# Performance work log

Hardware: AMD Instinct MI355X
Metric: run time of the kernel (lower is better)

Reference implementation:

```python
import jax, jax.numpy as jnp
import numpy as np


def setup_inputs() -> dict:
    key = jax.random.key(0)
    x = jax.random.normal(key, (4096, 512), dtype=jnp.float32)
    return {"x": x}


def reference(x):
    # Pairwise Euclidean distances for all (i, j) with i > j, flattened in the
    # same order as the original nested loop: (1,0),(2,0),(2,1),(3,0),...
    n = x.shape[0]
    sq = jnp.sum(x * x, axis=1)                      # [N]
    gram = x @ x.T                                   # [N, N]
    d2 = sq[:, None] + sq[None, :] - 2.0 * gram      # [N, N] squared dists
    ii, jj = jnp.tril_indices(n, k=-1)               # row-major lower triangle
    return jnp.sqrt(jnp.maximum(d2[ii, jj], 0.0))    # [N*(N-1)/2]
```

## Files before the change

kernel.cpp:

```cpp
#include <hip/hip_runtime.h>
#include <hip/hip_bf16.h>
#include <stdint.h>

#define N 4096
#define D 512
#define TILE 128
#define BK 128
#define KITERS (D / BK)
#define NB (N / TILE)

typedef float f32x4 __attribute__((ext_vector_type(4)));
typedef int   i32x8 __attribute__((ext_vector_type(8)));
typedef int   i32x4 __attribute__((ext_vector_type(4)));

__global__ __launch_bounds__(256) void prep_kernel(const float* __restrict__ x,
                                                   unsigned char* __restrict__ xq,
                                                   float* __restrict__ sq) {
    int row  = blockIdx.x * 4 + (threadIdx.x >> 6);
    int lane = threadIdx.x & 63;
    const float* xr = x + (size_t)row * D + lane * 8;
    float4 v0 = *reinterpret_cast<const float4*>(xr);
    float4 v1 = *reinterpret_cast<const float4*>(xr + 4);

    int w0 = __builtin_amdgcn_cvt_pk_fp8_f32(v0.x, v0.y, 0, false);
    w0     = __builtin_amdgcn_cvt_pk_fp8_f32(v0.z, v0.w, w0, true);
    int w1 = __builtin_amdgcn_cvt_pk_fp8_f32(v1.x, v1.y, 0, false);
    w1     = __builtin_amdgcn_cvt_pk_fp8_f32(v1.z, v1.w, w1, true);
    reinterpret_cast<int2*>(xq + (size_t)row * D)[lane] = make_int2(w0, w1);

    float s = v0.x * v0.x + v0.y * v0.y + v0.z * v0.z + v0.w * v0.w +
              v1.x * v1.x + v1.y * v1.y + v1.z * v1.z + v1.w * v1.w;
    #pragma unroll
    for (int off = 32; off > 0; off >>= 1) s += __shfl_down(s, off);
    if (lane == 0) sq[row] = s;
}

__global__ __launch_bounds__(256, 2) void pairdist_kernel(const unsigned char* __restrict__ xq,
                                                          const float* __restrict__ sq,
                                                          float* __restrict__ out) {
    __shared__ __align__(16) unsigned char As[TILE * BK];
    __shared__ __align__(16) unsigned char Bs[TILE * BK];

    int t  = blockIdx.x;
    int bi = (int)((sqrtf(8.0f * (float)t + 1.0f) - 1.0f) * 0.5f);
    while ((bi + 1) * (bi + 2) / 2 <= t) bi++;
    while (bi * (bi + 1) / 2 > t) bi--;
    int bj = t - bi * (bi + 1) / 2;

    int tid  = threadIdx.x;
    int w    = tid >> 6;
    int lane = tid & 63;
    int quad = lane >> 4;
    int lr   = lane & 15;
    int wm   = w >> 1;
    int wn   = w & 1;

    f32x4 acc[4][4];
    #pragma unroll
    for (int mt = 0; mt < 4; mt++)
        #pragma unroll
        for (int nt = 0; nt < 4; nt++)
            acc[mt][nt] = (f32x4)0.0f;

    int srow   = lane >> 3;
    int schunk = lane & 7;
    int sw     = ((schunk ^ srow) << 4);
    const unsigned char* ga = xq + (size_t)(bi * TILE + w * 32 + srow) * D + sw;
    const unsigned char* gb = xq + (size_t)(bj * TILE + w * 32 + srow) * D + sw;
    unsigned char* la = As + w * 32 * BK;
    unsigned char* lb = Bs + w * 32 * BK;

    for (int k0 = 0; k0 < D; k0 += BK) {
        __syncthreads();
        #pragma unroll
        for (int g = 0; g < 4; g++) {
            __builtin_amdgcn_global_load_lds(
                (const __attribute__((address_space(1))) void*)(ga + k0 + (size_t)g * 8 * D),
                (__attribute__((address_space(3))) void*)(la + g * 8 * BK), 16, 0, 0);
            __builtin_amdgcn_global_load_lds(
                (const __attribute__((address_space(1))) void*)(gb + k0 + (size_t)g * 8 * D),
                (__attribute__((address_space(3))) void*)(lb + g * 8 * BK), 16, 0, 0);
        }
        __syncthreads();

        int c0 = (((2 * quad) ^ (lr & 7)) << 4);
        int c1 = c0 ^ 16;
        i32x8 af[4], bfr[4];
        #pragma unroll
        for (int mt = 0; mt < 4; mt++) {
            const unsigned char* rb = As + (wm * 64 + mt * 16 + lr) * BK;
            i32x4 lo = *reinterpret_cast<const i32x4*>(rb + c0);
            i32x4 hi = *reinterpret_cast<const i32x4*>(rb + c1);
            af[mt][0] = lo[0]; af[mt][1] = lo[1]; af[mt][2] = lo[2]; af[mt][3] = lo[3];
            af[mt][4] = hi[0]; af[mt][5] = hi[1]; af[mt][6] = hi[2]; af[mt][7] = hi[3];
        }
        #pragma unroll
        for (int nt = 0; nt < 4; nt++) {
            const unsigned char* rb = Bs + (wn * 64 + nt * 16 + lr) * BK;
            i32x4 lo = *reinterpret_cast<const i32x4*>(rb + c0);
            i32x4 hi = *reinterpret_cast<const i32x4*>(rb + c1);
            bfr[nt][0] = lo[0]; bfr[nt][1] = lo[1]; bfr[nt][2] = lo[2]; bfr[nt][3] = lo[3];
            bfr[nt][4] = hi[0]; bfr[nt][5] = hi[1]; bfr[nt][6] = hi[2]; bfr[nt][7] = hi[3];
        }

        #pragma unroll
        for (int mt = 0; mt < 4; mt++)
            #pragma unroll
            for (int nt = 0; nt < 4; nt++)
                acc[mt][nt] = __builtin_amdgcn_mfma_scale_f32_16x16x128_f8f6f4(
                    af[mt], bfr[nt], acc[mt][nt],
                    0, 0,
                    0, 0x7F7F7F7F,
                    0, 0x7F7F7F7F);
    }

    int ibase = bi * TILE + wm * 64;
    int jbase = bj * TILE + wn * 64;

    float sqi[4][4], sqj[4];
    #pragma unroll
    for (int mt = 0; mt < 4; mt++)
        #pragma unroll
        for (int tt = 0; tt < 4; tt++)
            sqi[mt][tt] = sq[ibase + mt * 16 + quad * 4 + tt];
    #pragma unroll
    for (int nt = 0; nt < 4; nt++)
        sqj[nt] = sq[jbase + nt * 16 + lr];

    if (bi != bj) {
        #pragma unroll
        for (int mt = 0; mt < 4; mt++) {
            #pragma unroll
            for (int tt = 0; tt < 4; tt++) {
                int i = ibase + mt * 16 + quad * 4 + tt;
                unsigned rowoff = (unsigned)(i * (i - 1) / 2);
                #pragma unroll
                for (int nt = 0; nt < 4; nt++) {
                    int j = jbase + nt * 16 + lr;
                    float d2 = sqi[mt][tt] + sqj[nt] - 2.0f * acc[mt][nt][tt];
                    out[rowoff + (unsigned)j] = sqrtf(fmaxf(d2, 0.0f));
                }
            }
        }
    } else {
        #pragma unroll
        for (int mt = 0; mt < 4; mt++) {
            #pragma unroll
            for (int tt = 0; tt < 4; tt++) {
                int i = ibase + mt * 16 + quad * 4 + tt;
                unsigned rowoff = (unsigned)(i * (i - 1) / 2);
                #pragma unroll
                for (int nt = 0; nt < 4; nt++) {
                    int j = jbase + nt * 16 + lr;
                    if (j < i) {
                        float d2 = sqi[mt][tt] + sqj[nt] - 2.0f * acc[mt][nt][tt];
                        out[rowoff + (unsigned)j] = sqrtf(fmaxf(d2, 0.0f));
                    }
                }
            }
        }
    }
}

extern "C" void kernel_launch(void* const* d_in, const int* in_sizes, int n_in,
                              void* d_out, int out_size, void* d_ws, size_t ws_size,
                              hipStream_t stream) {
    const float* x = (const float*)d_in[0];
    float* out = (float*)d_out;

    unsigned char* xq = (unsigned char*)d_ws;
    float* sq = (float*)((char*)d_ws + (size_t)N * D);

    prep_kernel<<<N / 4, 256, 0, stream>>>(x, xq, sq);

    int nblocks = NB * (NB + 1) / 2;
    pairdist_kernel<<<nblocks, 256, 0, stream>>>(xq, sq, out);
}
```

Before: 81.07 us.

## Double-buffer LDS tiles, reorder diagonal blocks last, skip idle waves, nontemporal stores

Adds double-buffered LDS so the global-to-LDS loads for the next K chunk are issued before the MFMAs on the current chunk run. Off-diagonal tile blocks are scheduled first and diagonal blocks last, and on diagonal blocks the wave whose sub-tile lies entirely above the diagonal skips its MFMA work. The epilogue uses the hardware sqrt builtin and nontemporal stores for the large output write. LDS use per block doubles, which may limit occupancy.

Measured after the change: 93.27 us. +15.0%, slower.

```diff
diff --git a/kernel.cpp b/kernel.cpp
--- a/kernel.cpp
+++ b/kernel.cpp
@@ -1,5 +1,4 @@
 #include <hip/hip_runtime.h>
-#include <hip/hip_bf16.h>
 #include <stdint.h>
 
 #define N 4096
@@ -8,6 +7,8 @@
 #define BK 128
 #define KITERS (D / BK)
 #define NB (N / TILE)
+#define NOFF (NB * (NB - 1) / 2)
+#define NBLK (NB * (NB + 1) / 2)
 
 typedef float f32x4 __attribute__((ext_vector_type(4)));
 typedef int   i32x8 __attribute__((ext_vector_type(8)));
@@ -38,14 +39,19 @@
 __global__ __launch_bounds__(256, 2) void pairdist_kernel(const unsigned char* __restrict__ xq,
                                                           const float* __restrict__ sq,
                                                           float* __restrict__ out) {
-    __shared__ __align__(16) unsigned char As[TILE * BK];
-    __shared__ __align__(16) unsigned char Bs[TILE * BK];
-
-    int t  = blockIdx.x;
-    int bi = (int)((sqrtf(8.0f * (float)t + 1.0f) - 1.0f) * 0.5f);
-    while ((bi + 1) * (bi + 2) / 2 <= t) bi++;
-    while (bi * (bi + 1) / 2 > t) bi--;
-    int bj = t - bi * (bi + 1) / 2;
+    __shared__ __align__(16) unsigned char As[2][TILE * BK];
+    __shared__ __align__(16) unsigned char Bs[2][TILE * BK];
+
+    int t = blockIdx.x;
+    int bi, bj;
+    if (t >= NOFF) {
+        bi = bj = t - NOFF;
+    } else {
+        bi = (int)((sqrtf(8.0f * (float)t + 1.0f) + 1.0f) * 0.5f);
+        while (bi * (bi - 1) / 2 > t) bi--;
+        while ((bi + 1) * bi / 2 <= t) bi++;
+        bj = t - bi * (bi - 1) / 2;
+    }
 
     int tid  = threadIdx.x;
     int w    = tid >> 6;
@@ -55,68 +61,17 @@
     int wm   = w >> 1;
     int wn   = w & 1;
 
-    f32x4 acc[4][4];
-    #pragma unroll
-    for (int mt = 0; mt < 4; mt++)
-        #pragma unroll
-        for (int nt = 0; nt < 4; nt++)
-            acc[mt][nt] = (f32x4)0.0f;
+    const bool active = (bi != bj) || (wm >= wn);
 
     int srow   = lane >> 3;
     int schunk = lane & 7;
     int sw     = ((schunk ^ srow) << 4);
     const unsigned char* ga = xq + (size_t)(bi * TILE + w * 32 + srow) * D + sw;
     const unsigned char* gb = xq + (size_t)(bj * TILE + w * 32 + srow) * D + sw;
-    unsigned char* la = As + w * 32 * BK;
-    unsigned char* lb = Bs + w * 32 * BK;
-
-    for (int k0 = 0; k0 < D; k0 += BK) {
-        __syncthreads();
-        #pragma unroll
-        for (int g = 0; g < 4; g++) {
-            __builtin_amdgcn_global_load_lds(
-                (const __attribute__((address_space(1))) void*)(ga + k0 + (size_t)g * 8 * D),
-                (__attribute__((address_space(3))) void*)(la + g * 8 * BK), 16, 0, 0);
-            __builtin_amdgcn_global_load_lds(
-                (const __attribute__((address_space(1))) void*)(gb + k0 + (size_t)g * 8 * D),
-                (__attribute__((address_space(3))) void*)(lb + g * 8 * BK), 16, 0, 0);
-        }
-        __syncthreads();
-
-        int c0 = (((2 * quad) ^ (lr & 7)) << 4);
-        int c1 = c0 ^ 16;
-        i32x8 af[4], bfr[4];
-        #pragma unroll
-        for (int mt = 0; mt < 4; mt++) {
-            const unsigned char* rb = As + (wm * 64 + mt * 16 + lr) * BK;
-            i32x4 lo = *reinterpret_cast<const i32x4*>(rb + c0);
-            i32x4 hi = *reinterpret_cast<const i32x4*>(rb + c1);
-            af[mt][0] = lo[0]; af[mt][1] = lo[1]; af[mt][2] = lo[2]; af[mt][3] = lo[3];
-            af[mt][4] = hi[0]; af[mt][5] = hi[1]; af[mt][6] = hi[2]; af[mt][7] = hi[3];
-        }
-        #pragma unroll
-        for (int nt = 0; nt < 4; nt++) {
-            const unsigned char* rb = Bs + (wn * 64 + nt * 16 + lr) * BK;
-            i32x4 lo = *reinterpret_cast<const i32x4*>(rb + c0);
-            i32x4 hi = *reinterpret_cast<const i32x4*>(rb + c1);
-            bfr[nt][0] = lo[0]; bfr[nt][1] = lo[1]; bfr[nt][2] = lo[2]; bfr[nt][3] = lo[3];
-            bfr[nt][4] = hi[0]; bfr[nt][5] = hi[1]; bfr[nt][6] = hi[2]; bfr[nt][7] = hi[3];
-        }
-
-        #pragma unroll
-        for (int mt = 0; mt < 4; mt++)
-            #pragma unroll
-            for (int nt = 0; nt < 4; nt++)
-                acc[mt][nt] = __builtin_amdgcn_mfma_scale_f32_16x16x128_f8f6f4(
-                    af[mt], bfr[nt], acc[mt][nt],
-                    0, 0,
-                    0, 0x7F7F7F7F,
-                    0, 0x7F7F7F7F);
-    }
+    const int lbase = w * 32 * BK;
 
     int ibase = bi * TILE + wm * 64;
     int jbase = bj * TILE + wn * 64;
-
     float sqi[4][4], sqj[4];
     #pragma unroll
     for (int mt = 0; mt < 4; mt++)
@@ -126,6 +81,78 @@
     #pragma unroll
     for (int nt = 0; nt < 4; nt++)
         sqj[nt] = sq[jbase + nt * 16 + lr];
+
+    f32x4 acc[4][4];
+    #pragma unroll
+    for (int mt = 0; mt < 4; mt++)
+        #pragma unroll
+        for (int nt = 0; nt < 4; nt++)
+            acc[mt][nt] = (f32x4)0.0f;
+
+    #pragma unroll
+    for (int g = 0; g < 4; g++) {
+        __builtin_amdgcn_global_load_lds(
+            (const __attribute__((address_space(1))) void*)(ga + (size_t)g * 8 * D),
+            (__attribute__((address_space(3))) void*)(&As[0][lbase + g * 8 * BK]), 16, 0, 0);
+        __builtin_amdgcn_global_load_lds(
+            (const __attribute__((address_space(1))) void*)(gb + (size_t)g * 8 * D),
+            (__attribute__((address_space(3))) void*)(&Bs[0][lbase + g * 8 * BK]), 16, 0, 0);
+    }
+    __syncthreads();
+
+    #pragma unroll
+    for (int it = 0; it < KITERS; it++) {
+        const int curb = it & 1;
+
+        if (it + 1 < KITERS) {
+            const int nxt = curb ^ 1;
+            const int k0  = (it + 1) * BK;
+            #pragma unroll
+            for (int g = 0; g < 4; g++) {
+                __builtin_amdgcn_global_load_lds(
+                    (const __attribute__((address_space(1))) void*)(ga + k0 + (size_t)g * 8 * D),
+                    (__attribute__((address_space(3))) void*)(&As[nxt][lbase + g * 8 * BK]), 16, 0, 0);
+                __builtin_amdgcn_global_load_lds(
+                    (const __attribute__((address_space(1))) void*)(gb + k0 + (size_t)g * 8 * D),
+                    (__attribute__((address_space(3))) void*)(&Bs[nxt][lbase + g * 8 * BK]), 16, 0, 0);
+            }
+        }
+
+        if (active) {
+            int c0 = (((2 * quad) ^ (lr & 7)) << 4);
+            int c1 = c0 ^ 16;
+            i32x8 af[4], bfr[4];
+            #pragma unroll
+            for (int mt = 0; mt < 4; mt++) {
+                const unsigned char* rb = &As[curb][(wm * 64 + mt * 16 + lr) * BK];
+                i32x4 lo = *reinterpret_cast<const i32x4*>(rb + c0);
+                i32x4 hi = *reinterpret_cast<const i32x4*>(rb + c1);
+                af[mt][0] = lo[0]; af[mt][1] = lo[1]; af[mt][2] = lo[2]; af[mt][3] = lo[3];
+                af[mt][4] = hi[0]; af[mt][5] = hi[1]; af[mt][6] = hi[2]; af[mt][7] = hi[3];
+            }
+            #pragma unroll
+            for (int nt = 0; nt < 4; nt++) {
+                const unsigned char* rb = &Bs[curb][(wn * 64 + nt * 16 + lr) * BK];
+                i32x4 lo = *reinterpret_cast<const i32x4*>(rb + c0);
+                i32x4 hi = *reinterpret_cast<const i32x4*>(rb + c1);
+                bfr[nt][0] = lo[0]; bfr[nt][1] = lo[1]; bfr[nt][2] = lo[2]; bfr[nt][3] = lo[3];
+                bfr[nt][4] = hi[0]; bfr[nt][5] = hi[1]; bfr[nt][6] = hi[2]; bfr[nt][7] = hi[3];
+            }
+
+            #pragma unroll
+            for (int mt = 0; mt < 4; mt++)
+                #pragma unroll
+                for (int nt = 0; nt < 4; nt++)
+                    acc[mt][nt] = __builtin_amdgcn_mfma_scale_f32_16x16x128_f8f6f4(
+                        af[mt], bfr[nt], acc[mt][nt],
+                        0, 0,
+                        0, 0x7F7F7F7F,
+                        0, 0x7F7F7F7F);
+        }
+
+        if (it + 1 < KITERS)
+            __syncthreads();
+    }
 
     if (bi != bj) {
         #pragma unroll
@@ -138,7 +165,8 @@
                 for (int nt = 0; nt < 4; nt++) {
                     int j = jbase + nt * 16 + lr;
                     float d2 = sqi[mt][tt] + sqj[nt] - 2.0f * acc[mt][nt][tt];
-                    out[rowoff + (unsigned)j] = sqrtf(fmaxf(d2, 0.0f));
+                    float dd = __builtin_amdgcn_sqrtf(fmaxf(d2, 0.0f));
+                    __builtin_nontemporal_store(dd, &out[rowoff + (unsigned)j]);
                 }
             }
         }
@@ -154,7 +182,8 @@
                     int j = jbase + nt * 16 + lr;
                     if (j < i) {
                         float d2 = sqi[mt][tt] + sqj[nt] - 2.0f * acc[mt][nt][tt];
-                        out[rowoff + (unsigned)j] = sqrtf(fmaxf(d2, 0.0f));
+                        float dd = __builtin_amdgcn_sqrtf(fmaxf(d2, 0.0f));
+                        __builtin_nontemporal_store(dd, &out[rowoff + (unsigned)j]);
                     }
                 }
             }
@@ -173,6 +202,5 @@
 
     prep_kernel<<<N / 4, 256, 0, stream>>>(x, xq, sq);
 
-    int nblocks = NB * (NB + 1) / 2;
-    pairdist_kernel<<<nblocks, 256, 0, stream>>>(xq, sq, out);
+    pairdist_kernel<<<NBLK, 256, 0, stream>>>(xq, sq, out);
 }
```

## Reorder blocks, skip upper diagonal warp, cut registers, use raw sqrt

Applied to the files above, without the earlier changes.

Diagonal blocks are moved to the end of the grid and off-diagonal blocks use a revised triangular index map. On diagonal tiles the warp covering the upper triangle skips its LDS reads and MFMAs. A-fragment loading is interleaved with the MFMAs so fewer fragment registers are live, and launch bounds now target three blocks per CU instead of two. The square root uses the hardware builtin, which may be less precise than sqrtf, and the higher occupancy target may cause register spills.

Measured after the change: 79.59 us. No clear change (-1.8%).

```diff
diff --git a/kernel.cpp b/kernel.cpp
--- a/kernel.cpp
+++ b/kernel.cpp
@@ -1,5 +1,4 @@
 #include <hip/hip_runtime.h>
-#include <hip/hip_bf16.h>
 #include <stdint.h>
 
 #define N 4096
@@ -8,6 +7,8 @@
 #define BK 128
 #define KITERS (D / BK)
 #define NB (N / TILE)
+#define NOFF (NB * (NB - 1) / 2)
+#define NBLK (NB * (NB + 1) / 2)
 
 typedef float f32x4 __attribute__((ext_vector_type(4)));
 typedef int   i32x8 __attribute__((ext_vector_type(8)));
@@ -35,17 +36,22 @@
     if (lane == 0) sq[row] = s;
 }
 
-__global__ __launch_bounds__(256, 2) void pairdist_kernel(const unsigned char* __restrict__ xq,
+__global__ __launch_bounds__(256, 3) void pairdist_kernel(const unsigned char* __restrict__ xq,
                                                           const float* __restrict__ sq,
                                                           float* __restrict__ out) {
     __shared__ __align__(16) unsigned char As[TILE * BK];
     __shared__ __align__(16) unsigned char Bs[TILE * BK];
 
-    int t  = blockIdx.x;
-    int bi = (int)((sqrtf(8.0f * (float)t + 1.0f) - 1.0f) * 0.5f);
-    while ((bi + 1) * (bi + 2) / 2 <= t) bi++;
-    while (bi * (bi + 1) / 2 > t) bi--;
-    int bj = t - bi * (bi + 1) / 2;
+    int t = blockIdx.x;
+    int bi, bj;
+    if (t >= NOFF) {
+        bi = bj = t - NOFF;
+    } else {
+        bi = (int)((sqrtf(8.0f * (float)t + 1.0f) + 1.0f) * 0.5f);
+        while (bi * (bi - 1) / 2 > t) bi--;
+        while ((bi + 1) * bi / 2 <= t) bi++;
+        bj = t - bi * (bi - 1) / 2;
+    }
 
     int tid  = threadIdx.x;
     int w    = tid >> 6;
@@ -55,12 +61,7 @@
     int wm   = w >> 1;
     int wn   = w & 1;
 
-    f32x4 acc[4][4];
-    #pragma unroll
-    for (int mt = 0; mt < 4; mt++)
-        #pragma unroll
-        for (int nt = 0; nt < 4; nt++)
-            acc[mt][nt] = (f32x4)0.0f;
+    const bool active = (bi != bj) || (wm >= wn);
 
     int srow   = lane >> 3;
     int schunk = lane & 7;
@@ -69,6 +70,13 @@
     const unsigned char* gb = xq + (size_t)(bj * TILE + w * 32 + srow) * D + sw;
     unsigned char* la = As + w * 32 * BK;
     unsigned char* lb = Bs + w * 32 * BK;
+
+    f32x4 acc[4][4];
+    #pragma unroll
+    for (int mt = 0; mt < 4; mt++)
+        #pragma unroll
+        for (int nt = 0; nt < 4; nt++)
+            acc[mt][nt] = (f32x4)0.0f;
 
     for (int k0 = 0; k0 < D; k0 += BK) {
         __syncthreads();
@@ -83,35 +91,36 @@
         }
         __syncthreads();
 
-        int c0 = (((2 * quad) ^ (lr & 7)) << 4);
-        int c1 = c0 ^ 16;
-        i32x8 af[4], bfr[4];
-        #pragma unroll
-        for (int mt = 0; mt < 4; mt++) {
-            const unsigned char* rb = As + (wm * 64 + mt * 16 + lr) * BK;
-            i32x4 lo = *reinterpret_cast<const i32x4*>(rb + c0);
-            i32x4 hi = *reinterpret_cast<const i32x4*>(rb + c1);
-            af[mt][0] = lo[0]; af[mt][1] = lo[1]; af[mt][2] = lo[2]; af[mt][3] = lo[3];
-            af[mt][4] = hi[0]; af[mt][5] = hi[1]; af[mt][6] = hi[2]; af[mt][7] = hi[3];
+        if (active) {
+            int c0 = (((2 * quad) ^ (lr & 7)) << 4);
+            int c1 = c0 ^ 16;
+
+            i32x8 bfr[4];
+            #pragma unroll
+            for (int nt = 0; nt < 4; nt++) {
+                const unsigned char* rb = Bs + (wn * 64 + nt * 16 + lr) * BK;
+                i32x4 lo = *reinterpret_cast<const i32x4*>(rb + c0);
+                i32x4 hi = *reinterpret_cast<const i32x4*>(rb + c1);
+                bfr[nt][0] = lo[0]; bfr[nt][1] = lo[1]; bfr[nt][2] = lo[2]; bfr[nt][3] = lo[3];
+                bfr[nt][4] = hi[0]; bfr[nt][5] = hi[1]; bfr[nt][6] = hi[2]; bfr[nt][7] = hi[3];
+            }
+            #pragma unroll
+            for (int mt = 0; mt < 4; mt++) {
+                const unsigned char* rb = As + (wm * 64 + mt * 16 + lr) * BK;
+                i32x4 lo = *reinterpret_cast<const i32x4*>(rb + c0);
+                i32x4 hi = *reinterpret_cast<const i32x4*>(rb + c1);
+                i32x8 af;
+                af[0] = lo[0]; af[1] = lo[1]; af[2] = lo[2]; af[3] = lo[3];
+                af[4] = hi[0]; af[5] = hi[1]; af[6] = hi[2]; af[7] = hi[3];
+                #pragma unroll
+                for (int nt = 0; nt < 4; nt++)
+                    acc[mt][nt] = __builtin_amdgcn_mfma_scale_f32_16x16x128_f8f6f4(
+                        af, bfr[nt], acc[mt][nt],
+                        0, 0,
+                        0, 0x7F7F7F7F,
+                        0, 0x7F7F7F7F);
+            }
         }
-        #pragma unroll
-        for (int nt = 0; nt < 4; nt++) {
-            const unsigned char* rb = Bs + (wn * 64 + nt * 16 + lr) * BK;
-            i32x4 lo = *reinterpret_cast<const i32x4*>(rb + c0);
-            i32x4 hi = *reinterpret_cast<const i32x4*>(rb + c1);
-            bfr[nt][0] = lo[0]; bfr[nt][1] = lo[1]; bfr[nt][2] = lo[2]; bfr[nt][3] = lo[3];
-            bfr[nt][4] = hi[0]; bfr[nt][5] = hi[1]; bfr[nt][6] = hi[2]; bfr[nt][7] = hi[3];
-        }
-
-        #pragma unroll
-        for (int mt = 0; mt < 4; mt++)
-            #pragma unroll
-            for (int nt = 0; nt < 4; nt++)
-                acc[mt][nt] = __builtin_amdgcn_mfma_scale_f32_16x16x128_f8f6f4(
-                    af[mt], bfr[nt], acc[mt][nt],
-                    0, 0,
-                    0, 0x7F7F7F7F,
-                    0, 0x7F7F7F7F);
     }
 
     int ibase = bi * TILE + wm * 64;
@@ -138,7 +147,7 @@
                 for (int nt = 0; nt < 4; nt++) {
                     int j = jbase + nt * 16 + lr;
                     float d2 = sqi[mt][tt] + sqj[nt] - 2.0f * acc[mt][nt][tt];
-                    out[rowoff + (unsigned)j] = sqrtf(fmaxf(d2, 0.0f));
+                    out[rowoff + (unsigned)j] = __builtin_amdgcn_sqrtf(fmaxf(d2, 0.0f));
                 }
             }
         }
@@ -154,7 +163,7 @@
                     int j = jbase + nt * 16 + lr;
                     if (j < i) {
                         float d2 = sqi[mt][tt] + sqj[nt] - 2.0f * acc[mt][nt][tt];
-                        out[rowoff + (unsigned)j] = sqrtf(fmaxf(d2, 0.0f));
+                        out[rowoff + (unsigned)j] = __builtin_amdgcn_sqrtf(fmaxf(d2, 0.0f));
                     }
                 }
             }
@@ -173,6 +182,5 @@
 
     prep_kernel<<<N / 4, 256, 0, stream>>>(x, xq, sq);
 
-    int nblocks = NB * (NB + 1) / 2;
-    pairdist_kernel<<<nblocks, 256, 0, stream>>>(xq, sq, out);
+    pairdist_kernel<<<NBLK, 256, 0, stream>>>(xq, sq, out);
 }
```
